# Kernel tuning notes

Hardware: AMD Instinct MI355X
Metric: run time of the kernel (lower is better)

Reference implementation:

```python
import jax, jax.numpy as jnp
import numpy as np

NEG_SLOPE_ATT = 0.2   # GATConv attention leaky relu
NEG_SLOPE_ACT = 0.01  # F.leaky_relu default between layers


def gat_conv(x, src, dst, W, att_src, att_dst, bias, num_nodes):
    """PyG GATConv (concat=True, self-loops already in src/dst, no dropout at eval)."""
    H, C = att_src.shape
    h = (x @ W).reshape(num_nodes, H, C)            # [N,H,C]
    a_src = jnp.einsum('nhc,hc->nh', h, att_src)    # [N,H]
    a_dst = jnp.einsum('nhc,hc->nh', h, att_dst)
    e = jax.nn.leaky_relu(a_src[src] + a_dst[dst], NEG_SLOPE_ATT)  # [E,H]
    # segment softmax over incoming edges of each dst node
    m = jax.ops.segment_max(e, dst, num_segments=num_nodes)
    e = jnp.exp(e - m[dst])
    s = jax.ops.segment_sum(e, dst, num_segments=num_nodes)
    alpha = e / (s[dst] + 1e-16)                    # [E,H]
    msg = h[src] * alpha[..., None]                 # [E,H,C]
    out = jax.ops.segment_sum(msg, dst, num_segments=num_nodes)
    return out.reshape(num_nodes, H * C) + bias


def setup_inputs() -> dict:
    key = jax.random.key(0)
    ks = jax.random.split(key, 16)
    N, E = 50000, 1600000
    in_dim, hidden, heads, out_dim = 128, 32, 4, 64

    def glorot(k, shape):
        fan = shape[0] + shape[-1]
        return jax.random.uniform(k, shape, jnp.float32, -1.0, 1.0) * np.sqrt(6.0 / fan)

    x = jax.random.normal(ks[0], (N, in_dim), jnp.float32)
    edge_index = jax.random.randint(ks[1], (2, E), 0, N, jnp.int64)
    return {
        'x': x,
        'edge_index': edge_index,
        'W1': glorot(ks[2], (in_dim, heads * hidden)),
        'a1_src': glorot(ks[3], (heads, hidden)),
        'a1_dst': glorot(ks[4], (heads, hidden)),
        'b1': jnp.zeros((heads * hidden,), jnp.float32),
        'W2': glorot(ks[5], (heads * hidden, out_dim)),
        'a2_src': glorot(ks[6], (1, out_dim)),
        'a2_dst': glorot(ks[7], (1, out_dim)),
        'b2': jnp.zeros((out_dim,), jnp.float32),
        'Wd1': glorot(ks[8], (2 * out_dim, hidden)),
        'bd1': jnp.zeros((hidden,), jnp.float32),
        'Wd2': glorot(ks[9], (hidden, 1)),
        'bd2': jnp.zeros((1,), jnp.float32),
    }


def reference(x, edge_index, W1, a1_src, a1_dst, b1, W2, a2_src, a2_dst, b2,
              Wd1, bd1, Wd2, bd2):
    N = x.shape[0]
    # GATConv adds self-loops internally
    loops = jnp.arange(N, dtype=edge_index.dtype)
    src = jnp.concatenate([edge_index[0], loops])
    dst = jnp.concatenate([edge_index[1], loops])

    h1 = gat_conv(x, src, dst, W1, a1_src, a1_dst, b1, N)
    h1 = jax.nn.leaky_relu(h1, NEG_SLOPE_ACT)
    z = gat_conv(h1, src, dst, W2, a2_src, a2_dst, b2, N)

    # decoder: gather-concat-MLP over original edges
    feats = jnp.concatenate([z[edge_index[0]], z[edge_index[1]]], axis=1)  # [E,2*out]
    hdec = jax.nn.relu(feats @ Wd1 + bd1)
    edge_pred = hdec @ Wd2 + bd2                                           # [E,1]
    return edge_pred, z
```

## Files before the change

kernel.cpp:

```cpp
#include <hip/hip_runtime.h>
#include <hip/hip_bf16.h>
#include <math.h>

#define NEG_ATT 0.2f
#define NEG_ACT 0.01f
#define SHIFT_C 16.0f
#define CHUNK_E 8192
#define STAGE_MAX 12544

typedef __hip_bfloat16  bf16;
typedef unsigned short u16;
typedef short s8v __attribute__((ext_vector_type(8)));
typedef float f4v __attribute__((ext_vector_type(4)));

__device__ __forceinline__ float bflo(unsigned w) { return __uint_as_float(w << 16); }
__device__ __forceinline__ float bfhi(unsigned w) { return __uint_as_float(w & 0xFFFF0000u); }
__device__ __forceinline__ float lrelu_att(float a) { return fmaxf(a, NEG_ATT * a); }
__device__ __forceinline__ u16 f2b(float v) { bf16 h = __float2bfloat16(v); return *(u16*)&h; }

__global__ void k_histA(const int* __restrict__ ei, int E, int N, int* __restrict__ bhist) {
    __shared__ int h[256];
    h[threadIdx.x] = 0;
    __syncthreads();
    const long E2 = (long)E + N;
    for (long e = (long)blockIdx.x * blockDim.x + threadIdx.x; e < E2;
         e += (long)gridDim.x * blockDim.x) {
        int d = (e < E) ? ei[E + e] : (int)(e - E);
        atomicAdd(&h[d >> 8], 1);
    }
    __syncthreads();
    if (h[threadIdx.x]) atomicAdd(&bhist[threadIdx.x], h[threadIdx.x]);
}

__global__ void k_scanA(const int* __restrict__ bhist, int NBKT, int total,
                        int* __restrict__ bbase, int* __restrict__ bcur,
                        int* __restrict__ rowptr, int N) {
    __shared__ int ps[256];
    const int t = threadIdx.x;
    int v = (t < NBKT) ? bhist[t] : 0;
    ps[t] = v;
    __syncthreads();
    for (int off = 1; off < 256; off <<= 1) {
        int u = (t >= off) ? ps[t - off] : 0;
        __syncthreads();
        ps[t] += u;
        __syncthreads();
    }
    int ex = ps[t] - v;
    if (t < NBKT) { bbase[t] = ex; bcur[t] = ex; }
    if (t == 0) { bbase[NBKT] = total; rowptr[N] = total; }
}

__global__ void k_scatterA(const int* __restrict__ ei, int E, int N,
                           int* __restrict__ bcur, unsigned* __restrict__ pk) {
    __shared__ int cnt[256], offs[256], cur[256], gpos[256], ps[256];
    const int tid = threadIdx.x;
    const long E2 = (long)E + N;
    const long chunk0 = (long)blockIdx.x * CHUNK_E;
    const int cmax = (int)min((long)CHUNK_E, E2 - chunk0);
    cnt[tid] = 0;
    __syncthreads();
    for (int i = tid; i < cmax; i += 256) {
        long e = chunk0 + i;
        int d = (e < E) ? ei[E + e] : (int)(e - E);
        atomicAdd(&cnt[d >> 8], 1);
    }
    __syncthreads();
    int v = cnt[tid];
    ps[tid] = v;
    __syncthreads();
    for (int off = 1; off < 256; off <<= 1) {
        int u = (tid >= off) ? ps[tid - off] : 0;
        __syncthreads();
        ps[tid] += u;
        __syncthreads();
    }
    offs[tid] = ps[tid] - v;
    cur[tid]  = ps[tid] - v;
    gpos[tid] = atomicAdd(&bcur[tid], v);
    __syncthreads();
    for (int i = tid; i < cmax; i += 256) {
        long e = chunk0 + i;
        int d, s;
        if (e < E) { d = ei[E + e]; s = ei[e]; } else { d = s = (int)(e - E); }
        int b = d >> 8;
        int r = atomicAdd(&cur[b], 1);
        pk[gpos[b] + (r - offs[b])] = ((unsigned)(d & 255) << 16) | (unsigned)s;
    }
}

__global__ void k_scatterB(const unsigned* __restrict__ pk, const int* __restrict__ bbase,
                           int N, int* __restrict__ rowptr, u16* __restrict__ col) {
    __shared__ int hist[256], loff[256], lcur[256], ps[256];
    __shared__ u16 stage[STAGE_MAX];
    const int b = blockIdx.x;
    const int tid = threadIdx.x;
    const int ebeg = bbase[b], eend = bbase[b + 1];
    const int cnt = eend - ebeg;
    hist[tid] = 0;
    __syncthreads();
    for (int i = tid; i < cnt; i += 256) {
        unsigned p = pk[ebeg + i];
        atomicAdd(&hist[(p >> 16) & 255], 1);
    }
    __syncthreads();
    int v = hist[tid];
    ps[tid] = v;
    __syncthreads();
    for (int off = 1; off < 256; off <<= 1) {
        int u = (tid >= off) ? ps[tid - off] : 0;
        __syncthreads();
        ps[tid] += u;
        __syncthreads();
    }
    loff[tid] = ps[tid] - v;
    lcur[tid] = ps[tid] - v;
    const int n0 = b << 8;
    if (n0 + tid < N) rowptr[n0 + tid] = ebeg + loff[tid];
    __syncthreads();
    if (cnt <= STAGE_MAX) {
        for (int i = tid; i < cnt; i += 256) {
            unsigned p = pk[ebeg + i];
            int r = atomicAdd(&lcur[(p >> 16) & 255], 1);
            stage[r] = (u16)(p & 0xFFFFu);
        }
        __syncthreads();
        for (int i = tid; i < cnt; i += 256) col[ebeg + i] = stage[i];
    } else {
        for (int i = tid; i < cnt; i += 256) {
            unsigned p = pk[ebeg + i];
            int r = atomicAdd(&lcur[(p >> 16) & 255], 1);
            col[ebeg + r] = (u16)(p & 0xFFFFu);
        }
    }
}


__global__ void k_pack1(const float* __restrict__ W1, const float* __restrict__ a1sw,
                        const float* __restrict__ a1dw, u16* __restrict__ Wp) {
    const int total = 9 * 4 * 64 * 8;
    for (int i = blockIdx.x * blockDim.x + threadIdx.x; i < total; i += gridDim.x * blockDim.x) {
        int ct = i >> 11, rem = i & 2047;
        int kk = rem >> 9, l = (rem >> 3) & 63, j = i & 7;
        int k = kk * 32 + ((l >> 4) << 3) + j;
        int c = ct * 16 + (l & 15);
        float v = 0.f;
        if (c < 128) v = W1[k * 128 + c];
        else if (c < 132) {
            int h = c - 128;
            for (int q = 0; q < 32; ++q) v += W1[k * 128 + h * 32 + q] * a1sw[h * 32 + q];
        } else if (c < 136) {
            int h = c - 132;
            for (int q = 0; q < 32; ++q) v += W1[k * 128 + h * 32 + q] * a1dw[h * 32 + q];
        }
        Wp[i] = f2b(v);
    }
}

__global__ void k_pack2(const float* __restrict__ W2, const float* __restrict__ a2sw,
                        const float* __restrict__ a2dw, u16* __restrict__ Wp) {
    const int total = 5 * 4 * 64 * 8;
    for (int i = blockIdx.x * blockDim.x + threadIdx.x; i < total; i += gridDim.x * blockDim.x) {
        int ct = i >> 11, rem = i & 2047;
        int kk = rem >> 9, l = (rem >> 3) & 63, j = i & 7;
        int k = kk * 32 + ((l >> 4) << 3) + j;
        int c = ct * 16 + (l & 15);
        float v = 0.f;
        if (c < 64) v = W2[k * 64 + c];
        else if (c == 64) { for (int q = 0; q < 64; ++q) v += W2[k * 64 + q] * a2sw[q]; }
        else if (c == 65) { for (int q = 0; q < 64; ++q) v += W2[k * 64 + q] * a2dw[q]; }
        Wp[i] = f2b(v);
    }
}

__global__ void k_packd(const float* __restrict__ Wd1, u16* __restrict__ Wp) {
    const int total = 4 * 2 * 64 * 8;
    for (int i = blockIdx.x * blockDim.x + threadIdx.x; i < total; i += gridDim.x * blockDim.x) {
        int ct = i >> 10, rem = i & 1023;
        int kk = rem >> 9, l = (rem >> 3) & 63, j = i & 7;
        int k = kk * 32 + ((l >> 4) << 3) + j;
        int c = ct * 16 + (l & 15);
        float v = (c < 32) ? Wd1[k * 32 + c] : Wd1[(64 + k) * 32 + (c - 32)];
        Wp[i] = f2b(v);
    }
}

template<int MODE, int K, int CT>
__global__ void k_mfma(const float* __restrict__ in, const u16* __restrict__ Wp,
                       const float* __restrict__ bias,
                       bf16* __restrict__ ob, bf16* __restrict__ ob2,
                       float* __restrict__ o1, float* __restrict__ o2, int N) {
    constexpr int KK = K / 32;
    constexpr int KP = K + 8;
    __shared__ u16 As[64][KP];
    const int tid = threadIdx.x;
    const int w = tid >> 6, lane = tid & 63;
    const int row0 = blockIdx.x * 64;
    for (int i = tid; i < 64 * K; i += 256) {
        int rl = (K == 128) ? (i >> 7) : (i >> 6);
        int k  = i - rl * K;
        int n = row0 + rl;
        float v = (n < N) ? in[(size_t)n * K + k] : 0.f;
        if (MODE == 1) v = v > 0.f ? v : NEG_ACT * v;
        As[rl][k] = f2b(v);
    }
    __syncthreads();
    const int rloc = w * 16 + (lane & 15);
    const int kgrp = lane >> 4;
    s8v af[KK];
    #pragma unroll
    for (int kk = 0; kk < KK; ++kk)
        af[kk] = *(const s8v*)&As[rloc][kk * 32 + kgrp * 8];
    #pragma unroll
    for (int ct = 0; ct < CT; ++ct) {
        f4v acc = {0.f, 0.f, 0.f, 0.f};
        #pragma unroll
        for (int kk = 0; kk < KK; ++kk) {
            s8v b = *(const s8v*)&Wp[(size_t)((ct * KK + kk) * 64 + lane) * 8];
            acc = __builtin_amdgcn_mfma_f32_16x16x32_bf16(af[kk], b, acc, 0, 0, 0);
        }
        const int colb = ct * 16 + (lane & 15);
        #pragma unroll
        for (int r = 0; r < 4; ++r) {
            int n = row0 + w * 16 + kgrp * 4 + r;
            if (n >= N) continue;
            float val = acc[r];
            if (MODE == 0) {
                if (colb < 128)      ob[(size_t)n * 128 + colb] = __float2bfloat16(val);
                else if (colb < 132) o1[n * 4 + (colb - 128)] = val;
                else if (colb < 136) o2[n * 4 + (colb - 132)] = val;
            } else if (MODE == 1) {
                if (colb < 64)       ob[(size_t)n * 64 + colb] = __float2bfloat16(val);
                else if (colb == 64) o1[n] = val;
                else if (colb == 65) o2[n] = val;
            } else {
                if (colb < 32) ob[(size_t)n * 32 + colb] = __float2bfloat16(val + bias[colb]);
                else           ob2[(size_t)n * 32 + (colb - 32)] = __float2bfloat16(val);
            }
        }
    }
}

__global__ void k_aggr1(const int* __restrict__ rowptr, const u16* __restrict__ col,
                        const unsigned* __restrict__ h1q, const float* __restrict__ a1s,
                        const float* __restrict__ a1d, const float* __restrict__ b1,
                        float* __restrict__ g1, int N) {
    __shared__ float als[4][64][4];
    __shared__ int   scol[4][64];
    const int w = threadIdx.x >> 6;
    const int lane = threadIdx.x & 63;
    const int d = blockIdx.x * 4 + w;
    if (d >= N) return;
    const int lo = rowptr[d], hi = rowptr[d + 1];
    const float4 ad4 = *(const float4*)&a1d[d * 4];

    const int hh = lane >> 4;
    float acc0 = 0.f, acc1 = 0.f;
    float ws0 = 0.f, ws1 = 0.f, ws2 = 0.f, ws3 = 0.f;
    for (int base = lo; base < hi; base += 64) {
        const int cnt = min(64, hi - base);
        if (lane < cnt) {
            int s = col[base + lane];
            float4 as4 = *(const float4*)&a1s[s * 4];
            float a0 = lrelu_att(as4.x + ad4.x) - SHIFT_C;
            float a1 = lrelu_att(as4.y + ad4.y) - SHIFT_C;
            float a2 = lrelu_att(as4.z + ad4.z) - SHIFT_C;
            float a3 = lrelu_att(as4.w + ad4.w) - SHIFT_C;
            float4 al;
            al.x = __expf(a0); al.y = __expf(a1);
            al.z = __expf(a2); al.w = __expf(a3);
            ws0 += al.x; ws1 += al.y; ws2 += al.z; ws3 += al.w;
            *(float4*)&als[w][lane][0] = al;
            scol[w][lane] = s;
        }
        __builtin_amdgcn_wave_barrier();
        int t = 0;
        for (; t + 4 <= cnt; t += 4) {
            int s0 = scol[w][t], s1 = scol[w][t + 1], s2 = scol[w][t + 2], s3 = scol[w][t + 3];
            unsigned v0 = h1q[(((unsigned)s0) << 6) | (unsigned)lane];
            unsigned v1 = h1q[(((unsigned)s1) << 6) | (unsigned)lane];
            unsigned v2 = h1q[(((unsigned)s2) << 6) | (unsigned)lane];
            unsigned v3 = h1q[(((unsigned)s3) << 6) | (unsigned)lane];
            float al0 = als[w][t][hh],     al1 = als[w][t + 1][hh];
            float al2 = als[w][t + 2][hh], al3 = als[w][t + 3][hh];
            acc0 = fmaf(bflo(v0), al0, acc0); acc1 = fmaf(bfhi(v0), al0, acc1);
            acc0 = fmaf(bflo(v1), al1, acc0); acc1 = fmaf(bfhi(v1), al1, acc1);
            acc0 = fmaf(bflo(v2), al2, acc0); acc1 = fmaf(bfhi(v2), al2, acc1);
            acc0 = fmaf(bflo(v3), al3, acc0); acc1 = fmaf(bfhi(v3), al3, acc1);
        }
        for (; t < cnt; ++t) {
            int s = scol[w][t];
            float al = als[w][t][hh];
            unsigned v = h1q[(((unsigned)s) << 6) | (unsigned)lane];
            acc0 = fmaf(bflo(v), al, acc0);
            acc1 = fmaf(bfhi(v), al, acc1);
        }
        __builtin_amdgcn_wave_barrier();
    }
    #pragma unroll
    for (int off = 32; off >= 1; off >>= 1) {
        ws0 += __shfl_xor(ws0, off);
        ws1 += __shfl_xor(ws1, off);
        ws2 += __shfl_xor(ws2, off);
        ws3 += __shfl_xor(ws3, off);
    }
    float wsel = (hh == 0) ? ws0 : (hh == 1) ? ws1 : (hh == 2) ? ws2 : ws3;
    float inv = 1.f / (wsel + 1e-16f);
    float2 outv;
    outv.x = acc0 * inv + b1[2 * lane];
    outv.y = acc1 * inv + b1[2 * lane + 1];
    *(float2*)&g1[(long)d * 128 + 2 * lane] = outv;
}

__global__ void k_aggr2(const int* __restrict__ rowptr, const u16* __restrict__ col,
                        const unsigned short* __restrict__ h2s, const float* __restrict__ a2s,
                        const float* __restrict__ a2d, const float* __restrict__ b2,
                        float* __restrict__ zout, int N) {
    __shared__ float als[4][64];
    __shared__ int   scol[4][64];
    const int w = threadIdx.x >> 6;
    const int lane = threadIdx.x & 63;
    const int d = blockIdx.x * 4 + w;
    if (d >= N) return;
    const int lo = rowptr[d], hi = rowptr[d + 1];
    const float ad = a2d[d];

    float acc = 0.f, wsum = 0.f;
    for (int base = lo; base < hi; base += 64) {
        const int cnt = min(64, hi - base);
        if (lane < cnt) {
            int s = col[base + lane];
            float a = lrelu_att(a2s[s] + ad) - SHIFT_C;
            float al = __expf(a);
            wsum += al;
            als[w][lane] = al;
            scol[w][lane] = s;
        }
        __builtin_amdgcn_wave_barrier();
        int t = 0;
        for (; t + 4 <= cnt; t += 4) {
            int s0 = scol[w][t], s1 = scol[w][t + 1], s2 = scol[w][t + 2], s3 = scol[w][t + 3];
            float v0 = __uint_as_float((unsigned)h2s[(((unsigned)s0) << 6) | (unsigned)lane] << 16);
            float v1 = __uint_as_float((unsigned)h2s[(((unsigned)s1) << 6) | (unsigned)lane] << 16);
            float v2 = __uint_as_float((unsigned)h2s[(((unsigned)s2) << 6) | (unsigned)lane] << 16);
            float v3 = __uint_as_float((unsigned)h2s[(((unsigned)s3) << 6) | (unsigned)lane] << 16);
            acc = fmaf(v0, als[w][t], acc);
            acc = fmaf(v1, als[w][t + 1], acc);
            acc = fmaf(v2, als[w][t + 2], acc);
            acc = fmaf(v3, als[w][t + 3], acc);
        }
        for (; t < cnt; ++t) {
            int s = scol[w][t];
            float v = __uint_as_float((unsigned)h2s[(((unsigned)s) << 6) | (unsigned)lane] << 16);
            acc = fmaf(v, als[w][t], acc);
        }
        __builtin_amdgcn_wave_barrier();
    }
    #pragma unroll
    for (int off = 32; off >= 1; off >>= 1) wsum += __shfl_xor(wsum, off);
    zout[(long)d * 64 + lane] = acc / (wsum + 1e-16f) + b2[lane];
}

__global__ void k_dec2(const int* __restrict__ ei, int E,
                       const bf16* __restrict__ u, const bf16* __restrict__ v,
                       const float* __restrict__ Wd2, const float* __restrict__ bd2,
                       float* __restrict__ pred) {
    const int g = threadIdx.x >> 3;
    const int l = threadIdx.x & 7;
    long e = (long)blockIdx.x * 32 + g;
    if (e >= E) return;
    int s = ei[e], d = ei[E + e];
    uint2 ua = *(const uint2*)(u + (long)s * 32 + l * 4);
    uint2 vb = *(const uint2*)(v + (long)d * 32 + l * 4);
    float4 wv = *(const float4*)&Wd2[l * 4];
    float h0 = fmaxf(bflo(ua.x) + bflo(vb.x), 0.f);
    float h1 = fmaxf(bfhi(ua.x) + bfhi(vb.x), 0.f);
    float h2 = fmaxf(bflo(ua.y) + bflo(vb.y), 0.f);
    float h3 = fmaxf(bfhi(ua.y) + bfhi(vb.y), 0.f);
    float p = h0 * wv.x;
    p = fmaf(h1, wv.y, p);
    p = fmaf(h2, wv.z, p);
    p = fmaf(h3, wv.w, p);
    p += __shfl_xor(p, 1, 8);
    p += __shfl_xor(p, 2, 8);
    p += __shfl_xor(p, 4, 8);
    if (l == 0) pred[e] = p + bd2[0];
}

extern "C" void kernel_launch(void* const* d_in, const int* in_sizes, int n_in,
                              void* d_out, int out_size, void* d_ws, size_t ws_size,
                              hipStream_t stream) {
    const float* x    = (const float*)d_in[0];
    const int*   ei   = (const int*)d_in[1];
    const float* W1   = (const float*)d_in[2];
    const float* a1sw = (const float*)d_in[3];
    const float* a1dw = (const float*)d_in[4];
    const float* b1   = (const float*)d_in[5];
    const float* W2   = (const float*)d_in[6];
    const float* a2sw = (const float*)d_in[7];
    const float* a2dw = (const float*)d_in[8];
    const float* b2   = (const float*)d_in[9];
    const float* Wd1  = (const float*)d_in[10];
    const float* bd1  = (const float*)d_in[11];
    const float* Wd2  = (const float*)d_in[12];
    const float* bd2  = (const float*)d_in[13];

    const int N = in_sizes[0] / 128;
    const int E = in_sizes[1] / 2;
    const int E2 = E + N;
    const int NBKT = (N + 255) >> 8;

    float* pred = (float*)d_out;
    float* zout = (float*)d_out + E;

    float* W = (float*)d_ws;
    size_t o = 0;
    float* g1  = W + o; o += (size_t)N * 128;
    bf16* h1b  = (bf16*)(W + o); o += (size_t)N * 64;
    bf16* h2b  = (bf16*)(W + o); o += (size_t)N * 32;
    bf16* ub   = (bf16*)(W + o); o += (size_t)N * 16;
    bf16* vb   = (bf16*)(W + o); o += (size_t)N * 16;
    float* a1s = W + o; o += (size_t)N * 4;
    float* a1d = W + o; o += (size_t)N * 4;
    float* a2s = W + o; o += (size_t)N;
    float* a2d = W + o; o += (size_t)N;
    int* rowptr = (int*)(W + o); o += (size_t)N + 1;
    unsigned* pk = (unsigned*)(W + o); o += (size_t)E2;
    u16* col    = (u16*)(W + o); o += ((size_t)E2 + 1) / 2;
    int* bhist  = (int*)(W + o); o += 257;
    int* bbase  = (int*)(W + o); o += 257;
    int* bcur   = (int*)(W + o); o += 257;
    u16* Wp1   = (u16*)(W + o); o += 9216;
    u16* Wp2   = (u16*)(W + o); o += 5120;
    u16* Wpd   = (u16*)(W + o); o += 2048;
    if (ws_size < o * sizeof(float)) return;

    const int TB = 256;
    const int NBLK = (N + 63) >> 6;

    k_pack1<<<16, TB, 0, stream>>>(W1, a1sw, a1dw, Wp1);
    k_pack2<<<16, TB, 0, stream>>>(W2, a2sw, a2dw, Wp2);
    k_packd<<<16, TB, 0, stream>>>(Wd1, Wpd);

    hipMemsetAsync(bhist, 0, 257 * sizeof(int), stream);
    k_histA<<<512, TB, 0, stream>>>(ei, E, N, bhist);
    k_scanA<<<1, TB, 0, stream>>>(bhist, NBKT, E2, bbase, bcur, rowptr, N);
    k_scatterA<<<(E2 + CHUNK_E - 1) / CHUNK_E, TB, 0, stream>>>(ei, E, N, bcur, pk);
    k_scatterB<<<NBKT, TB, 0, stream>>>(pk, bbase, N, rowptr, col);

    k_mfma<0, 128, 9><<<NBLK, TB, 0, stream>>>(x, Wp1, bd1, h1b, h1b, a1s, a1d, N);
    k_aggr1<<<(N + 3) / 4, TB, 0, stream>>>(rowptr, col, (const unsigned*)h1b, a1s, a1d, b1, g1, N);

    k_mfma<1, 128, 5><<<NBLK, TB, 0, stream>>>(g1, Wp2, bd1, h2b, h2b, a2s, a2d, N);
    k_aggr2<<<(N + 3) / 4, TB, 0, stream>>>(rowptr, col, (const unsigned short*)h2b, a2s, a2d, b2, zout, N);

    k_mfma<2, 64, 4><<<NBLK, TB, 0, stream>>>(zout, Wpd, bd1, ub, vb, a1s, a1d, N);
    k_dec2<<<(E + 31) / 32, TB, 0, stream>>>(ei, E, ub, vb, Wd2, bd2, pred);
}
```

Before: 267.2 us.

## Store layer-1 output in bf16, merge pack kernels, deepen gather unroll, two edges per decoder group

The layer-1 aggregation now writes its output as packed bf16 instead of fp32, and the second projection reads it as bf16. This halves that intermediate's write and read traffic. The three weight-packing kernels are merged into one launch. The gather loops in both aggregation kernels are unrolled by 8 instead of 4 to keep more loads in flight. The decoder processes two edges per 8-lane group, halving the grid size. The bf16 intermediate was already rounded to bf16 at the MFMA input, so its effect on accuracy should be small.

```diff
diff --git a/kernel.cpp b/kernel.cpp
--- a/kernel.cpp
+++ b/kernel.cpp
@@ -135,58 +135,56 @@
     }
 }
 
-
-__global__ void k_pack1(const float* __restrict__ W1, const float* __restrict__ a1sw,
-                        const float* __restrict__ a1dw, u16* __restrict__ Wp) {
-    const int total = 9 * 4 * 64 * 8;
-    for (int i = blockIdx.x * blockDim.x + threadIdx.x; i < total; i += gridDim.x * blockDim.x) {
-        int ct = i >> 11, rem = i & 2047;
-        int kk = rem >> 9, l = (rem >> 3) & 63, j = i & 7;
-        int k = kk * 32 + ((l >> 4) << 3) + j;
-        int c = ct * 16 + (l & 15);
-        float v = 0.f;
-        if (c < 128) v = W1[k * 128 + c];
-        else if (c < 132) {
-            int h = c - 128;
-            for (int q = 0; q < 32; ++q) v += W1[k * 128 + h * 32 + q] * a1sw[h * 32 + q];
-        } else if (c < 136) {
-            int h = c - 132;
-            for (int q = 0; q < 32; ++q) v += W1[k * 128 + h * 32 + q] * a1dw[h * 32 + q];
-        }
-        Wp[i] = f2b(v);
-    }
-}
-
-__global__ void k_pack2(const float* __restrict__ W2, const float* __restrict__ a2sw,
-                        const float* __restrict__ a2dw, u16* __restrict__ Wp) {
-    const int total = 5 * 4 * 64 * 8;
-    for (int i = blockIdx.x * blockDim.x + threadIdx.x; i < total; i += gridDim.x * blockDim.x) {
-        int ct = i >> 11, rem = i & 2047;
-        int kk = rem >> 9, l = (rem >> 3) & 63, j = i & 7;
-        int k = kk * 32 + ((l >> 4) << 3) + j;
-        int c = ct * 16 + (l & 15);
-        float v = 0.f;
-        if (c < 64) v = W2[k * 64 + c];
-        else if (c == 64) { for (int q = 0; q < 64; ++q) v += W2[k * 64 + q] * a2sw[q]; }
-        else if (c == 65) { for (int q = 0; q < 64; ++q) v += W2[k * 64 + q] * a2dw[q]; }
-        Wp[i] = f2b(v);
-    }
-}
-
-__global__ void k_packd(const float* __restrict__ Wd1, u16* __restrict__ Wp) {
-    const int total = 4 * 2 * 64 * 8;
-    for (int i = blockIdx.x * blockDim.x + threadIdx.x; i < total; i += gridDim.x * blockDim.x) {
-        int ct = i >> 10, rem = i & 1023;
-        int kk = rem >> 9, l = (rem >> 3) & 63, j = i & 7;
-        int k = kk * 32 + ((l >> 4) << 3) + j;
-        int c = ct * 16 + (l & 15);
-        float v = (c < 32) ? Wd1[k * 32 + c] : Wd1[(64 + k) * 32 + (c - 32)];
-        Wp[i] = f2b(v);
-    }
-}
-
-template<int MODE, int K, int CT>
-__global__ void k_mfma(const float* __restrict__ in, const u16* __restrict__ Wp,
+__global__ void k_pack(const float* __restrict__ W1, const float* __restrict__ a1sw,
+                       const float* __restrict__ a1dw,
+                       const float* __restrict__ W2, const float* __restrict__ a2sw,
+                       const float* __restrict__ a2dw,
+                       const float* __restrict__ Wd1,
+                       u16* __restrict__ Wp1, u16* __restrict__ Wp2, u16* __restrict__ Wpd) {
+    const int T1 = 9 * 4 * 64 * 8, T2 = 5 * 4 * 64 * 8, TD = 4 * 2 * 64 * 8;
+    for (int gi = blockIdx.x * blockDim.x + threadIdx.x; gi < T1 + T2 + TD;
+         gi += gridDim.x * blockDim.x) {
+        if (gi < T1) {
+            int i = gi;
+            int ct = i >> 11, rem = i & 2047;
+            int kk = rem >> 9, l = (rem >> 3) & 63, j = i & 7;
+            int k = kk * 32 + ((l >> 4) << 3) + j;
+            int c = ct * 16 + (l & 15);
+            float v = 0.f;
+            if (c < 128) v = W1[k * 128 + c];
+            else if (c < 132) {
+                int h = c - 128;
+                for (int q = 0; q < 32; ++q) v += W1[k * 128 + h * 32 + q] * a1sw[h * 32 + q];
+            } else if (c < 136) {
+                int h = c - 132;
+                for (int q = 0; q < 32; ++q) v += W1[k * 128 + h * 32 + q] * a1dw[h * 32 + q];
+            }
+            Wp1[i] = f2b(v);
+        } else if (gi < T1 + T2) {
+            int i = gi - T1;
+            int ct = i >> 11, rem = i & 2047;
+            int kk = rem >> 9, l = (rem >> 3) & 63, j = i & 7;
+            int k = kk * 32 + ((l >> 4) << 3) + j;
+            int c = ct * 16 + (l & 15);
+            float v = 0.f;
+            if (c < 64) v = W2[k * 64 + c];
+            else if (c == 64) { for (int q = 0; q < 64; ++q) v += W2[k * 64 + q] * a2sw[q]; }
+            else if (c == 65) { for (int q = 0; q < 64; ++q) v += W2[k * 64 + q] * a2dw[q]; }
+            Wp2[i] = f2b(v);
+        } else {
+            int i = gi - T1 - T2;
+            int ct = i >> 10, rem = i & 1023;
+            int kk = rem >> 9, l = (rem >> 3) & 63, j = i & 7;
+            int k = kk * 32 + ((l >> 4) << 3) + j;
+            int c = ct * 16 + (l & 15);
+            float v = (c < 32) ? Wd1[k * 32 + c] : Wd1[(64 + k) * 32 + (c - 32)];
+            Wpd[i] = f2b(v);
+        }
+    }
+}
+
+template<int MODE, int K, int CT, int INBF>
+__global__ void k_mfma(const void* __restrict__ in_, const u16* __restrict__ Wp,
                        const float* __restrict__ bias,
                        bf16* __restrict__ ob, bf16* __restrict__ ob2,
                        float* __restrict__ o1, float* __restrict__ o2, int N) {
@@ -200,7 +198,11 @@
         int rl = (K == 128) ? (i >> 7) : (i >> 6);
         int k  = i - rl * K;
         int n = row0 + rl;
-        float v = (n < N) ? in[(size_t)n * K + k] : 0.f;
+        float v = 0.f;
+        if (n < N) {
+            if (INBF) v = __uint_as_float((unsigned)((const u16*)in_)[(size_t)n * K + k] << 16);
+            else      v = ((const float*)in_)[(size_t)n * K + k];
+        }
         if (MODE == 1) v = v > 0.f ? v : NEG_ACT * v;
         As[rl][k] = f2b(v);
     }
@@ -244,7 +246,7 @@
 __global__ void k_aggr1(const int* __restrict__ rowptr, const u16* __restrict__ col,
                         const unsigned* __restrict__ h1q, const float* __restrict__ a1s,
                         const float* __restrict__ a1d, const float* __restrict__ b1,
-                        float* __restrict__ g1, int N) {
+                        unsigned* __restrict__ g1b, int N) {
     __shared__ float als[4][64][4];
     __shared__ int   scol[4][64];
     const int w = threadIdx.x >> 6;
@@ -275,18 +277,20 @@
         }
         __builtin_amdgcn_wave_barrier();
         int t = 0;
-        for (; t + 4 <= cnt; t += 4) {
-            int s0 = scol[w][t], s1 = scol[w][t + 1], s2 = scol[w][t + 2], s3 = scol[w][t + 3];
-            unsigned v0 = h1q[(((unsigned)s0) << 6) | (unsigned)lane];
-            unsigned v1 = h1q[(((unsigned)s1) << 6) | (unsigned)lane];
-            unsigned v2 = h1q[(((unsigned)s2) << 6) | (unsigned)lane];
-            unsigned v3 = h1q[(((unsigned)s3) << 6) | (unsigned)lane];
-            float al0 = als[w][t][hh],     al1 = als[w][t + 1][hh];
-            float al2 = als[w][t + 2][hh], al3 = als[w][t + 3][hh];
-            acc0 = fmaf(bflo(v0), al0, acc0); acc1 = fmaf(bfhi(v0), al0, acc1);
-            acc0 = fmaf(bflo(v1), al1, acc0); acc1 = fmaf(bfhi(v1), al1, acc1);
-            acc0 = fmaf(bflo(v2), al2, acc0); acc1 = fmaf(bfhi(v2), al2, acc1);
-            acc0 = fmaf(bflo(v3), al3, acc0); acc1 = fmaf(bfhi(v3), al3, acc1);
+        for (; t + 8 <= cnt; t += 8) {
+            unsigned vv[8];
+            float aa[8];
+            #pragma unroll
+            for (int q = 0; q < 8; ++q) {
+                int s = scol[w][t + q];
+                vv[q] = h1q[(((unsigned)s) << 6) | (unsigned)lane];
+                aa[q] = als[w][t + q][hh];
+            }
+            #pragma unroll
+            for (int q = 0; q < 8; ++q) {
+                acc0 = fmaf(bflo(vv[q]), aa[q], acc0);
+                acc1 = fmaf(bfhi(vv[q]), aa[q], acc1);
+            }
         }
         for (; t < cnt; ++t) {
             int s = scol[w][t];
@@ -306,10 +310,9 @@
     }
     float wsel = (hh == 0) ? ws0 : (hh == 1) ? ws1 : (hh == 2) ? ws2 : ws3;
     float inv = 1.f / (wsel + 1e-16f);
-    float2 outv;
-    outv.x = acc0 * inv + b1[2 * lane];
-    outv.y = acc1 * inv + b1[2 * lane + 1];
-    *(float2*)&g1[(long)d * 128 + 2 * lane] = outv;
+    unsigned outw = ((unsigned)f2b(acc1 * inv + b1[2 * lane + 1]) << 16)
+                  | (unsigned)f2b(acc0 * inv + b1[2 * lane]);
+    g1b[(size_t)d * 64 + lane] = outw;
 }
 
 __global__ void k_aggr2(const int* __restrict__ rowptr, const u16* __restrict__ col,
@@ -338,16 +341,16 @@
         }
         __builtin_amdgcn_wave_barrier();
         int t = 0;
-        for (; t + 4 <= cnt; t += 4) {
-            int s0 = scol[w][t], s1 = scol[w][t + 1], s2 = scol[w][t + 2], s3 = scol[w][t + 3];
-            float v0 = __uint_as_float((unsigned)h2s[(((unsigned)s0) << 6) | (unsigned)lane] << 16);
-            float v1 = __uint_as_float((unsigned)h2s[(((unsigned)s1) << 6) | (unsigned)lane] << 16);
-            float v2 = __uint_as_float((unsigned)h2s[(((unsigned)s2) << 6) | (unsigned)lane] << 16);
-            float v3 = __uint_as_float((unsigned)h2s[(((unsigned)s3) << 6) | (unsigned)lane] << 16);
-            acc = fmaf(v0, als[w][t], acc);
-            acc = fmaf(v1, als[w][t + 1], acc);
-            acc = fmaf(v2, als[w][t + 2], acc);
-            acc = fmaf(v3, als[w][t + 3], acc);
+        for (; t + 8 <= cnt; t += 8) {
+            float vv[8], aa[8];
+            #pragma unroll
+            for (int q = 0; q < 8; ++q) {
+                int s = scol[w][t + q];
+                vv[q] = __uint_as_float((unsigned)h2s[(((unsigned)s) << 6) | (unsigned)lane] << 16);
+                aa[q] = als[w][t + q];
+            }
+            #pragma unroll
+            for (int q = 0; q < 8; ++q) acc = fmaf(vv[q], aa[q], acc);
         }
         for (; t < cnt; ++t) {
             int s = scol[w][t];
@@ -367,24 +370,49 @@
                        float* __restrict__ pred) {
     const int g = threadIdx.x >> 3;
     const int l = threadIdx.x & 7;
-    long e = (long)blockIdx.x * 32 + g;
-    if (e >= E) return;
-    int s = ei[e], d = ei[E + e];
-    uint2 ua = *(const uint2*)(u + (long)s * 32 + l * 4);
-    uint2 vb = *(const uint2*)(v + (long)d * 32 + l * 4);
+    long e0 = (long)blockIdx.x * 64 + g * 2;
+    if (e0 >= E) return;
+    long e1 = e0 + 1;
+    const bool has1 = (e1 < E);
+    int s0 = ei[e0], d0 = ei[E + e0];
+    int s1 = has1 ? (int)ei[e1] : s0;
+    int d1 = has1 ? (int)ei[E + e1] : d0;
+    uint2 ua0 = *(const uint2*)(u + (long)s0 * 32 + l * 4);
+    uint2 vb0 = *(const uint2*)(v + (long)d0 * 32 + l * 4);
+    uint2 ua1 = *(const uint2*)(u + (long)s1 * 32 + l * 4);
+    uint2 vb1 = *(const uint2*)(v + (long)d1 * 32 + l * 4);
     float4 wv = *(const float4*)&Wd2[l * 4];
-    float h0 = fmaxf(bflo(ua.x) + bflo(vb.x), 0.f);
-    float h1 = fmaxf(bfhi(ua.x) + bfhi(vb.x), 0.f);
-    float h2 = fmaxf(bflo(ua.y) + bflo(vb.y), 0.f);
-    float h3 = fmaxf(bfhi(ua.y) + bfhi(vb.y), 0.f);
-    float p = h0 * wv.x;
-    p = fmaf(h1, wv.y, p);
-    p = fmaf(h2, wv.z, p);
-    p = fmaf(h3, wv.w, p);
-    p += __shfl_xor(p, 1, 8);
-    p += __shfl_xor(p, 2, 8);
-    p += __shfl_xor(p, 4, 8);
-    if (l == 0) pred[e] = p + bd2[0];
+    float p0, p1;
+    {
+        float h0 = fmaxf(bflo(ua0.x) + bflo(vb0.x), 0.f);
+        float h1 = fmaxf(bfhi(ua0.x) + bfhi(vb0.x), 0.f);
+        float h2 = fmaxf(bflo(ua0.y) + bflo(vb0.y), 0.f);
+        float h3 = fmaxf(bfhi(ua0.y) + bfhi(vb0.y), 0.f);
+        p0 = h0 * wv.x;
+        p0 = fmaf(h1, wv.y, p0);
+        p0 = fmaf(h2, wv.z, p0);
+        p0 = fmaf(h3, wv.w, p0);
+    }
+    {
+        float h0 = fmaxf(bflo(ua1.x) + bflo(vb1.x), 0.f);
+        float h1 = fmaxf(bfhi(ua1.x) + bfhi(vb1.x), 0.f);
+        float h2 = fmaxf(bflo(ua1.y) + bflo(vb1.y), 0.f);
+        float h3 = fmaxf(bfhi(ua1.y) + bfhi(vb1.y), 0.f);
+        p1 = h0 * wv.x;
+        p1 = fmaf(h1, wv.y, p1);
+        p1 = fmaf(h2, wv.z, p1);
+        p1 = fmaf(h3, wv.w, p1);
+    }
+    p0 += __shfl_xor(p0, 1, 8);
+    p0 += __shfl_xor(p0, 2, 8);
+    p0 += __shfl_xor(p0, 4, 8);
+    p1 += __shfl_xor(p1, 1, 8);
+    p1 += __shfl_xor(p1, 2, 8);
+    p1 += __shfl_xor(p1, 4, 8);
+    if (l == 0) {
+        pred[e0] = p0 + bd2[0];
+        if (has1) pred[e1] = p1 + bd2[0];
+    }
 }
 
 extern "C" void kernel_launch(void* const* d_in, const int* in_sizes, int n_in,
@@ -415,7 +443,7 @@
 
     float* W = (float*)d_ws;
     size_t o = 0;
-    float* g1  = W + o; o += (size_t)N * 128;
+    unsigned* g1b = (unsigned*)(W + o); o += (size_t)N * 64;
     bf16* h1b  = (bf16*)(W + o); o += (size_t)N * 64;
     bf16* h2b  = (bf16*)(W + o); o += (size_t)N * 32;
     bf16* ub   = (bf16*)(W + o); o += (size_t)N * 16;
@@ -438,9 +466,7 @@
     const int TB = 256;
     const int NBLK = (N + 63) >> 6;
 
-    k_pack1<<<16, TB, 0, stream>>>(W1, a1sw, a1dw, Wp1);
-    k_pack2<<<16, TB, 0, stream>>>(W2, a2sw, a2dw, Wp2);
-    k_packd<<<16, TB, 0, stream>>>(Wd1, Wpd);
+    k_pack<<<48, TB, 0, stream>>>(W1, a1sw, a1dw, W2, a2sw, a2dw, Wd1, Wp1, Wp2, Wpd);
 
     hipMemsetAsync(bhist, 0, 257 * sizeof(int), stream);
     k_histA<<<512, TB, 0, stream>>>(ei, E, N, bhist);
@@ -448,12 +474,12 @@
     k_scatterA<<<(E2 + CHUNK_E - 1) / CHUNK_E, TB, 0, stream>>>(ei, E, N, bcur, pk);
     k_scatterB<<<NBKT, TB, 0, stream>>>(pk, bbase, N, rowptr, col);
 
-    k_mfma<0, 128, 9><<<NBLK, TB, 0, stream>>>(x, Wp1, bd1, h1b, h1b, a1s, a1d, N);
-    k_aggr1<<<(N + 3) / 4, TB, 0, stream>>>(rowptr, col, (const unsigned*)h1b, a1s, a1d, b1, g1, N);
-
-    k_mfma<1, 128, 5><<<NBLK, TB, 0, stream>>>(g1, Wp2, bd1, h2b, h2b, a2s, a2d, N);
+    k_mfma<0, 128, 9, 0><<<NBLK, TB, 0, stream>>>(x, Wp1, bd1, h1b, h1b, a1s, a1d, N);
+    k_aggr1<<<(N + 3) / 4, TB, 0, stream>>>(rowptr, col, (const unsigned*)h1b, a1s, a1d, b1, g1b, N);
+
+    k_mfma<1, 128, 5, 1><<<NBLK, TB, 0, stream>>>(g1b, Wp2, bd1, h2b, h2b, a2s, a2d, N);
     k_aggr2<<<(N + 3) / 4, TB, 0, stream>>>(rowptr, col, (const unsigned short*)h2b, a2s, a2d, b2, zout, N);
 
-    k_mfma<2, 64, 4><<<NBLK, TB, 0, stream>>>(zout, Wpd, bd1, ub, vb, a1s, a1d, N);
-    k_dec2<<<(E + 31) / 32, TB, 0, stream>>>(ei, E, ub, vb, Wd2, bd2, pred);
-}
+    k_mfma<2, 64, 4, 0><<<NBLK, TB, 0, stream>>>(zout, Wpd, bd1, ub, vb, a1s, a1d, N);
+    k_dec2<<<(E + 63) / 64, TB, 0, stream>>>(ei, E, ub, vb, Wd2, bd2, pred);
+}
```

Result: faster. 251.6 us (-5.8%).
